# Kernel optimization log

Hardware: AMD Instinct MI355X
Metric: run time of the kernel (lower is better)

## Reference

```python
import jax, jax.numpy as jnp
import numpy as np
from jax import lax

N, C_IN, C_OUT = 1, 16, 32
D = W = H = 48
K = 9                      # num_points (snake kernel size)
CENTER = K // 2
EXTEND_SCOPE = 1.0
EPS = 1e-5
GN_GROUPS = C_OUT // 4
DN = ('NCDHW', 'OIDHW', 'NCDHW')


def conv3d(x, w, strides, padding):
    return lax.conv_general_dilated(x, w, strides, padding, dimension_numbers=DN)


def snake_cumsum(off):
    # off: [N, K, D, W, H]. Cumulative offsets outward from the center point,
    # center forced to 0 (matches the sequential loop in _coordinate_map_3D).
    lower = jnp.flip(jnp.cumsum(jnp.flip(off[:, :CENTER], 1), 1), 1)
    upper = jnp.cumsum(off[:, CENTER + 1:], 1)
    zero = jnp.zeros_like(off[:, :1])
    return jnp.concatenate([lower, zero, upper], axis=1)


def coordinate_map_morph0(off):
    # off: [N, 6K, D, W, H]; morph==0 uses z_offset1 (chans [0,K)) and y_offset1 ([K,2K)).
    cz = snake_cumsum(off[:, :K])
    cy = snake_cumsum(off[:, K:2 * K])
    dt = off.dtype
    zb = jnp.arange(D, dtype=dt)[None, None, :, None, None]
    yb = jnp.arange(W, dtype=dt)[None, None, None, :, None]
    xb = (jnp.arange(H, dtype=dt)[None, None, None, None, :]
          + (jnp.arange(K, dtype=dt) - CENTER)[None, :, None, None, None])
    z = zb + EXTEND_SCOPE * cz                      # [N,K,D,W,H]
    y = yb + EXTEND_SCOPE * cy
    x = jnp.broadcast_to(xb, z.shape)

    def rearr(c):  # [N,K,D,W,H] -> [N,D,W,H*K]  (h-major, k-minor, as in torch permute/reshape)
        return jnp.transpose(c, (0, 2, 3, 4, 1)).reshape(c.shape[0], D, W, H * K)

    return rearr(z), rearr(y), rearr(x)


def trilinear(feat, z, y, x):
    # feat [N,C,D,W,H]; z,y,x [N,D,W,H*K] float coords -> [N,C,D,W,H*K]
    z = jnp.clip(z, 0.0, D - 1.0)
    y = jnp.clip(y, 0.0, W - 1.0)
    x = jnp.clip(x, 0.0, H - 1.0)
    z0 = jnp.clip(jnp.floor(z).astype(jnp.int32), 0, D - 1); z1 = jnp.clip(z0 + 1, 0, D - 1)
    y0 = jnp.clip(jnp.floor(y).astype(jnp.int32), 0, W - 1); y1 = jnp.clip(y0 + 1, 0, W - 1)
    x0 = jnp.clip(jnp.floor(x).astype(jnp.int32), 0, H - 1); x1 = jnp.clip(x0 + 1, 0, H - 1)
    featl = jnp.transpose(feat, (0, 2, 3, 4, 1))  # [N,D,W,H,C]
    b = jnp.arange(feat.shape[0])[:, None, None, None]
    g = lambda zi, yi, xi: featl[b, zi, yi, xi]   # [N,D,W,H*K,C]
    f = feat.dtype
    wz0 = (z1.astype(f) - z)[..., None]; wz1 = (z - z0.astype(f))[..., None]
    wy0 = (y1.astype(f) - y)[..., None]; wy1 = (y - y0.astype(f))[..., None]
    wx0 = (x1.astype(f) - x)[..., None]; wx1 = (x - x0.astype(f))[..., None]
    out = (g(z0, y0, x0) * wz0 * wy0 * wx0 + g(z0, y0, x1) * wz0 * wy0 * wx1
         + g(z0, y1, x0) * wz0 * wy1 * wx0 + g(z0, y1, x1) * wz0 * wy1 * wx1
         + g(z1, y0, x0) * wz1 * wy0 * wx0 + g(z1, y0, x1) * wz1 * wy0 * wx1
         + g(z1, y1, x0) * wz1 * wy1 * wx0 + g(z1, y1, x1) * wz1 * wy1 * wx1)
    return jnp.transpose(out, (0, 4, 1, 2, 3))


def group_norm(x, gamma, beta):
    n = x.shape[0]
    xg = x.reshape(n, GN_GROUPS, -1)
    mu = xg.mean(-1, keepdims=True)
    var = xg.var(-1, keepdims=True)
    xg = (xg - mu) * lax.rsqrt(var + EPS)
    return xg.reshape(x.shape) * gamma[None, :, None, None, None] + beta[None, :, None, None, None]


def setup_inputs() -> dict:
    key = jax.random.key(0)
    ks = jax.random.split(key, 6)
    s = 0.05
    return {
        'x': jax.random.normal(ks[0], (N, C_IN, D, W, H), jnp.float32),
        'ow': jax.random.normal(ks[1], (6 * K, C_IN, 3, 3, 3), jnp.float32) * s,
        'ob': jax.random.normal(ks[2], (6 * K,), jnp.float32) * s,
        'bn_gamma': jnp.ones((6 * K,), jnp.float32),
        'bn_beta': jnp.zeros((6 * K,), jnp.float32),
        'bn_mean': jnp.zeros((6 * K,), jnp.float32),
        'bn_var': jnp.ones((6 * K,), jnp.float32),
        'dw': jax.random.normal(ks[3], (C_OUT, C_IN, 1, 1, K), jnp.float32) * s,
        'db': jax.random.normal(ks[4], (C_OUT,), jnp.float32) * s,
        'gn_gamma': jnp.ones((C_OUT,), jnp.float32),
        'gn_beta': jnp.zeros((C_OUT,), jnp.float32),
    }


def reference(x, ow, ob, bn_gamma, bn_beta, bn_mean, bn_var, dw, db, gn_gamma, gn_beta):
    # offset branch: conv3x3x3 -> BN (eval) -> tanh
    off = conv3d(x, ow, (1, 1, 1), 'SAME') + ob[None, :, None, None, None]
    c = lambda v: v[None, :, None, None, None]
    off = (off - c(bn_mean)) * lax.rsqrt(c(bn_var) + EPS) * c(bn_gamma) + c(bn_beta)
    off = jnp.tanh(off)
    # deformed sampling coordinates (morph 0: spread along x/height axis)
    zc, yc, xc = coordinate_map_morph0(off)
    deformed = trilinear(x, zc, yc, xc)           # [N,C,D,W,H*K]
    # snake conv: kernel (1,1,K) stride (1,1,K) -> [N,C_OUT,D,W,H]
    out = conv3d(deformed, dw, (1, 1, K), 'VALID') + db[None, :, None, None, None]
    out = group_norm(out, gn_gamma, gn_beta)
    return jax.nn.relu(out)
```

## Files before the change

### kernel.cpp

```cpp
#include <hip/hip_runtime.h>

#define DD    48
#define SP    (48*48*48)
#define CIN   16
#define KOFF  18
#define COUT  32
#define KK    9
#define NG    8
#define EPSV  1e-5f

__global__ __launch_bounds__(256) void k_zero(float* __restrict__ stats) {
    stats[threadIdx.x] = 0.0f;
}

__global__ __launch_bounds__(256) void k_xt(const float* __restrict__ x,
                                            float* __restrict__ xt) {
    int t = threadIdx.x;
    int vb = t >> 2, c = t & 3;
    int v = blockIdx.x * 64 + vb;
    float4 o;
    o.x = x[(4 * c + 0) * SP + v];
    o.y = x[(4 * c + 1) * SP + v];
    o.z = x[(4 * c + 2) * SP + v];
    o.w = x[(4 * c + 3) * SP + v];
    *reinterpret_cast<float4*>(xt + v * 16 + 4 * c) = o;
}

#define COH 9
__global__ __launch_bounds__(256) void k_offset(
    const float* __restrict__ xt, const float* __restrict__ ow,
    const float* __restrict__ ob, const float* __restrict__ bng,
    const float* __restrict__ bnb,const float* __restrict__ bnm,
    const float* __restrict__ bnv,float* __restrict__ off)
{
    const int cb = blockIdx.y * COH;
    __shared__ float wsm[27 * 4 * COH * 4];
    for (int i = threadIdx.x; i < 27 * CIN * COH; i += 256) {
        int co = i % COH; int r = i / COH; int ci = r % CIN; int tap = r / CIN;
        int c = ci >> 2, j = ci & 3;
        wsm[((tap * 4 + c) * COH + co) * 4 + j] = ow[((cb + co) * CIN + ci) * 27 + tap];
    }
    __syncthreads();

    const int t  = threadIdx.x;
    const int c  = t & 3;
    const int vb = t >> 2;
    const int v  = blockIdx.x * 64 + vb;
    const int h = v % DD, w = (v / DD) % DD, d = v / (DD * DD);

    float acc[COH];
#pragma unroll
    for (int co = 0; co < COH; ++co) acc[co] = 0.0f;

    const float* xc = xt + 4 * c;

#pragma unroll
    for (int kd = 0; kd < 3; ++kd) {
        int z = d + kd - 1; bool okz = (unsigned)z < (unsigned)DD;
#pragma unroll
        for (int kw = 0; kw < 3; ++kw) {
            int yy = w + kw - 1; bool oky = (unsigned)yy < (unsigned)DD;
#pragma unroll
            for (int kh = 0; kh < 3; ++kh) {
                int xx = h + kh - 1;
                if (okz && oky && (unsigned)xx < (unsigned)DD) {
                    int tap = (kd * 3 + kw) * 3 + kh;
                    float4 xv = *reinterpret_cast<const float4*>(
                        xc + ((z * DD + yy) * DD + xx) * 16);
                    const float4* wrow = reinterpret_cast<const float4*>(
                        &wsm[(tap * 4 + c) * COH * 4]);
#pragma unroll
                    for (int co = 0; co < COH; ++co) {
                        float4 w4 = wrow[co];
                        acc[co] += w4.x * xv.x + w4.y * xv.y
                                 + w4.z * xv.z + w4.w * xv.w;
                    }
                }
            }
        }
    }

#pragma unroll
    for (int co = 0; co < COH; ++co) {
        acc[co] += __shfl_xor(acc[co], 1);
        acc[co] += __shfl_xor(acc[co], 2);
    }

#pragma unroll
    for (int c0 = 0; c0 < 3; ++c0) {
        if (c == c0) {
#pragma unroll
            for (int j = 0; j < 3; ++j) {
                int co = c0 * 3 + j;
                int ch = cb + co;
                float scale = bng[ch] * rsqrtf(bnv[ch] + EPSV);
                float val   = (acc[co] + ob[ch] - bnm[ch]) * scale + bnb[ch];
                off[ch * SP + v] = tanhf(val);
            }
        }
    }
}

__global__ __launch_bounds__(256) void k_snake(
    const float* __restrict__ xt,  const float* __restrict__ off,
    const float* __restrict__ dw,  const float* __restrict__ db,
    float* __restrict__ pre,       float* __restrict__ stats)
{
    __shared__ float wl[KK * 4 * 132];
    __shared__ float lstat[16];
    for (int i = threadIdx.x; i < KK * CIN * COUT; i += 256) {
        int co = i % COUT; int r = i / COUT; int ci = r % CIN; int k = r / CIN;
        int c = ci >> 2, j = ci & 3;
        wl[(k * 4 + c) * 132 + co * 4 + j] = dw[(co * CIN + ci) * KK + k];
    }
    if (threadIdx.x < 16) lstat[threadIdx.x] = 0.0f;
    __syncthreads();

    const int nwg = SP / 64;
    int bid = (int)blockIdx.x;
    bid = (bid & 7) * (nwg >> 3) + (bid >> 3);

    const int t  = threadIdx.x;
    const int c  = t & 3;
    const int vb = t >> 2;
    const int v  = bid * 64 + vb;
    const int h = v % DD, w = (v / DD) % DD, d = v / (DD * DD);

    float acc[COUT];
#pragma unroll
    for (int co = 0; co < COUT; ++co) acc[co] = 0.0f;

    auto process = [&](int k, float czv, float cyv) {
        int xcol = h + k - 4;
        if (xcol >= DD - 1) return;
        if (xcol < 0) xcol = 0;

        float zf = fminf(fmaxf((float)d + czv, 0.0f), 47.0f);
        float yf = fminf(fmaxf((float)w + cyv, 0.0f), 47.0f);
        int z0 = (int)zf, y0 = (int)yf;
        int z1 = min(z0 + 1, 47), y1 = min(y0 + 1, 47);
        float wz1 = zf - (float)z0, wz0 = (float)z1 - zf;
        float wy1 = yf - (float)y0, wy0 = (float)y1 - yf;
        float w00 = wz0 * wy0, w01 = wz0 * wy1, w10 = wz1 * wy0, w11 = wz1 * wy1;

        const float* base = xt + 4 * c;
        float s0, s1, s2, s3;
        {
            const float4 A = *reinterpret_cast<const float4*>(base + ((z0 * DD + y0) * DD + xcol) * 16);
            const float4 B = *reinterpret_cast<const float4*>(base + ((z0 * DD + y1) * DD + xcol) * 16);
            s0 = w00 * A.x + w01 * B.x;
            s1 = w00 * A.y + w01 * B.y;
            s2 = w00 * A.z + w01 * B.z;
            s3 = w00 * A.w + w01 * B.w;
        }
        {
            const float4 C = *reinterpret_cast<const float4*>(base + ((z1 * DD + y0) * DD + xcol) * 16);
            const float4 E = *reinterpret_cast<const float4*>(base + ((z1 * DD + y1) * DD + xcol) * 16);
            s0 += w10 * C.x + w11 * E.x;
            s1 += w10 * C.y + w11 * E.y;
            s2 += w10 * C.z + w11 * E.z;
            s3 += w10 * C.w + w11 * E.w;
        }

        const float4* wrow = reinterpret_cast<const float4*>(&wl[(k * 4 + c) * 132]);
#pragma unroll
        for (int co = 0; co < COUT; ++co) {
            float4 w4 = wrow[co];
            acc[co] += w4.x * s0 + w4.y * s1 + w4.z * s2 + w4.w * s3;
        }
    };

    process(4, 0.0f, 0.0f);
    {
        float rz = 0.0f, ry = 0.0f;
#pragma unroll
        for (int k = 3; k >= 0; --k) {
            rz += off[k * SP + v];
            ry += off[(KK + k) * SP + v];
            process(k, rz, ry);
        }
    }
    {
        float rz = 0.0f, ry = 0.0f;
#pragma unroll
        for (int k = 5; k < KK; ++k) {
            rz += off[k * SP + v];
            ry += off[(KK + k) * SP + v];
            process(k, rz, ry);
        }
    }

#pragma unroll
    for (int co = 0; co < COUT; ++co) {
        acc[co] += __shfl_xor(acc[co], 1);
        acc[co] += __shfl_xor(acc[co], 2);
        acc[co] += db[co];
    }

#pragma unroll
    for (int cc = 0; cc < 4; ++cc) {
        if (c == cc) {
#pragma unroll
            for (int j = 0; j < 8; ++j)
                pre[(cc * 8 + j) * SP + v] = acc[cc * 8 + j];
        }
    }

#pragma unroll
    for (int g = 0; g < NG; ++g) {
        float a0 = acc[4*g], a1 = acc[4*g+1], a2 = acc[4*g+2], a3 = acc[4*g+3];
        float s  = a0 + a1 + a2 + a3;
        float ss = a0*a0 + a1*a1 + a2*a2 + a3*a3;
#pragma unroll
        for (int o = 4; o <= 32; o <<= 1) {
            s  += __shfl_xor(s,  o);
            ss += __shfl_xor(ss, o);
        }
        if ((t & 63) == 0) {
            atomicAdd(&lstat[g],      s);
            atomicAdd(&lstat[NG + g], ss);
        }
    }
    __syncthreads();
    if (t < 16) atomicAdd(&stats[t * 16], lstat[t]);
}

__global__ __launch_bounds__(256) void k_gn(
    float* __restrict__ buf, const float* __restrict__ stats,
    const float* __restrict__ gamma, const float* __restrict__ beta)
{
    int idx  = blockIdx.x * 256 + threadIdx.x;
    int base = idx * 4;
    int ch = base / SP, g = ch >> 2;

    const float inv_n = 1.0f / (4.0f * (float)SP);
    float mean = stats[g * 16] * inv_n;
    float var  = stats[(NG + g) * 16] * inv_n - mean * mean;
    float rs   = rsqrtf(var + EPSV);
    float ga   = gamma[ch] * rs;
    float be   = beta[ch] - mean * ga;

    float4 p = *reinterpret_cast<const float4*>(buf + base);
    float4 o;
    o.x = fmaxf(p.x * ga + be, 0.0f);
    o.y = fmaxf(p.y * ga + be, 0.0f);
    o.z = fmaxf(p.z * ga + be, 0.0f);
    o.w = fmaxf(p.w * ga + be, 0.0f);
    *reinterpret_cast<float4*>(buf + base) = o;
}

extern "C" void kernel_launch(void* const* d_in, const int* in_sizes, int n_in,
                              void* d_out, int out_size, void* d_ws, size_t ws_size,
                              hipStream_t stream)
{
    const float* x   = (const float*)d_in[0];
    const float* ow  = (const float*)d_in[1];
    const float* ob  = (const float*)d_in[2];
    const float* bng = (const float*)d_in[3];
    const float* bnb = (const float*)d_in[4];
    const float* bnm = (const float*)d_in[5];
    const float* bnv = (const float*)d_in[6];
    const float* dw  = (const float*)d_in[7];
    const float* db  = (const float*)d_in[8];
    const float* gng = (const float*)d_in[9];
    const float* gnb = (const float*)d_in[10];
    float* out = (float*)d_out;

    float* off   = (float*)d_ws;
    float* xt    = off + KOFF * SP;
    float* stats = xt + CIN * SP;

    k_zero  <<<1, 256, 0, stream>>>(stats);
    k_xt    <<<SP / 64, 256, 0, stream>>>(x, xt);
    k_offset<<<dim3(SP / 64, 2), 256, 0, stream>>>(xt, ow, ob, bng, bnb, bnm, bnv, off);
    k_snake <<<SP / 64, 256, 0, stream>>>(xt, off, dw, db, out, stats);
    k_gn    <<<(COUT * SP / 4) / 256, 256, 0, stream>>>(out, stats, gng, gnb);
}
```

Before: 224.7 us.

## Fuse offset conv with snake sampling to keep offsets in registers

Merges the offset convolution/BN/tanh kernel into the snake deformable-sampling kernel so the 18 offset channels stay in registers instead of going through a global workspace. Per-channel BN scale and shift are also precomputed once per block in shared memory. This removes the offset tensor's global write and read and one kernel launch. In exchange it raises register and LDS use per block, which may lower occupancy.

Result: slower. 283.0 us (+25.9%).

```diff
diff --git a/kernel.cpp b/kernel.cpp
--- a/kernel.cpp
+++ b/kernel.cpp
@@ -3,7 +3,6 @@
 #define DD    48
 #define SP    (48*48*48)
 #define CIN   16
-#define KOFF  18
 #define COUT  32
 #define KK    9
 #define NG    8
@@ -26,33 +25,53 @@
     *reinterpret_cast<float4*>(xt + v * 16 + 4 * c) = o;
 }
 
-#define COH 9
-__global__ __launch_bounds__(256) void k_offset(
-    const float* __restrict__ xt, const float* __restrict__ ow,
-    const float* __restrict__ ob, const float* __restrict__ bng,
-    const float* __restrict__ bnb,const float* __restrict__ bnm,
-    const float* __restrict__ bnv,float* __restrict__ off)
+__global__ __launch_bounds__(256) void k_fused(
+    const float* __restrict__ xt,  const float* __restrict__ ow,
+    const float* __restrict__ ob,  const float* __restrict__ bng,
+    const float* __restrict__ bnb, const float* __restrict__ bnm,
+    const float* __restrict__ bnv, const float* __restrict__ dw,
+    const float* __restrict__ db,  float* __restrict__ pre,
+    float* __restrict__ stats)
 {
-    const int cb = blockIdx.y * COH;
-    __shared__ float wsm[27 * 4 * COH * 4];
-    for (int i = threadIdx.x; i < 27 * CIN * COH; i += 256) {
-        int co = i % COH; int r = i / COH; int ci = r % CIN; int tap = r / CIN;
+    __shared__ float cw[27 * 4 * 72];
+    __shared__ float wl[KK * 4 * 132];
+    __shared__ float bnsc[18], bnsh[18];
+    __shared__ float lstat[16];
+
+    for (int i = threadIdx.x; i < 27 * CIN * 18; i += 256) {
+        int ch = i % 18; int r = i / 18; int ci = r % CIN; int tap = r / CIN;
         int c = ci >> 2, j = ci & 3;
-        wsm[((tap * 4 + c) * COH + co) * 4 + j] = ow[((cb + co) * CIN + ci) * 27 + tap];
-    }
+        cw[(tap * 4 + c) * 72 + ch * 4 + j] = ow[(ch * CIN + ci) * 27 + tap];
+    }
+    for (int i = threadIdx.x; i < KK * CIN * COUT; i += 256) {
+        int co = i % COUT; int r = i / COUT; int ci = r % CIN; int k = r / CIN;
+        int c = ci >> 2, j = ci & 3;
+        wl[(k * 4 + c) * 132 + co * 4 + j] = dw[(co * CIN + ci) * KK + k];
+    }
+    if (threadIdx.x < 18) {
+        int ch = threadIdx.x;
+        float sc = bng[ch] * rsqrtf(bnv[ch] + EPSV);
+        bnsc[ch] = sc;
+        bnsh[ch] = (ob[ch] - bnm[ch]) * sc + bnb[ch];
+    }
+    if (threadIdx.x < 16) lstat[threadIdx.x] = 0.0f;
     __syncthreads();
+
+    const int nwg = SP / 64;
+    int bid = (int)blockIdx.x;
+    bid = (bid & 7) * (nwg >> 3) + (bid >> 3);
 
     const int t  = threadIdx.x;
     const int c  = t & 3;
     const int vb = t >> 2;
-    const int v  = blockIdx.x * 64 + vb;
+    const int v  = bid * 64 + vb;
     const int h = v % DD, w = (v / DD) % DD, d = v / (DD * DD);
 
-    float acc[COH];
-#pragma unroll
-    for (int co = 0; co < COH; ++co) acc[co] = 0.0f;
-
     const float* xc = xt + 4 * c;
+
+    float a18[18];
+#pragma unroll
+    for (int co = 0; co < 18; ++co) a18[co] = 0.0f;
 
 #pragma unroll
     for (int kd = 0; kd < 3; ++kd) {
@@ -68,11 +87,11 @@
                     float4 xv = *reinterpret_cast<const float4*>(
                         xc + ((z * DD + yy) * DD + xx) * 16);
                     const float4* wrow = reinterpret_cast<const float4*>(
-                        &wsm[(tap * 4 + c) * COH * 4]);
-#pragma unroll
-                    for (int co = 0; co < COH; ++co) {
+                        &cw[(tap * 4 + c) * 72]);
+#pragma unroll
+                    for (int co = 0; co < 18; ++co) {
                         float4 w4 = wrow[co];
-                        acc[co] += w4.x * xv.x + w4.y * xv.y
+                        a18[co] += w4.x * xv.x + w4.y * xv.y
                                  + w4.z * xv.z + w4.w * xv.w;
                     }
                 }
@@ -81,50 +100,11 @@
     }
 
 #pragma unroll
-    for (int co = 0; co < COH; ++co) {
-        acc[co] += __shfl_xor(acc[co], 1);
-        acc[co] += __shfl_xor(acc[co], 2);
-    }
-
-#pragma unroll
-    for (int c0 = 0; c0 < 3; ++c0) {
-        if (c == c0) {
-#pragma unroll
-            for (int j = 0; j < 3; ++j) {
-                int co = c0 * 3 + j;
-                int ch = cb + co;
-                float scale = bng[ch] * rsqrtf(bnv[ch] + EPSV);
-                float val   = (acc[co] + ob[ch] - bnm[ch]) * scale + bnb[ch];
-                off[ch * SP + v] = tanhf(val);
-            }
-        }
-    }
-}
-
-__global__ __launch_bounds__(256) void k_snake(
-    const float* __restrict__ xt,  const float* __restrict__ off,
-    const float* __restrict__ dw,  const float* __restrict__ db,
-    float* __restrict__ pre,       float* __restrict__ stats)
-{
-    __shared__ float wl[KK * 4 * 132];
-    __shared__ float lstat[16];
-    for (int i = threadIdx.x; i < KK * CIN * COUT; i += 256) {
-        int co = i % COUT; int r = i / COUT; int ci = r % CIN; int k = r / CIN;
-        int c = ci >> 2, j = ci & 3;
-        wl[(k * 4 + c) * 132 + co * 4 + j] = dw[(co * CIN + ci) * KK + k];
-    }
-    if (threadIdx.x < 16) lstat[threadIdx.x] = 0.0f;
-    __syncthreads();
-
-    const int nwg = SP / 64;
-    int bid = (int)blockIdx.x;
-    bid = (bid & 7) * (nwg >> 3) + (bid >> 3);
-
-    const int t  = threadIdx.x;
-    const int c  = t & 3;
-    const int vb = t >> 2;
-    const int v  = bid * 64 + vb;
-    const int h = v % DD, w = (v / DD) % DD, d = v / (DD * DD);
+    for (int co = 0; co < 18; ++co) {
+        a18[co] += __shfl_xor(a18[co], 1);
+        a18[co] += __shfl_xor(a18[co], 2);
+        a18[co] = tanhf(a18[co] * bnsc[co] + bnsh[co]);
+    }
 
     float acc[COUT];
 #pragma unroll
@@ -175,8 +155,8 @@
         float rz = 0.0f, ry = 0.0f;
 #pragma unroll
         for (int k = 3; k >= 0; --k) {
-            rz += off[k * SP + v];
-            ry += off[(KK + k) * SP + v];
+            rz += a18[k];
+            ry += a18[KK + k];
             process(k, rz, ry);
         }
     }
@@ -184,8 +164,8 @@
         float rz = 0.0f, ry = 0.0f;
 #pragma unroll
         for (int k = 5; k < KK; ++k) {
-            rz += off[k * SP + v];
-            ry += off[(KK + k) * SP + v];
+            rz += a18[k];
+            ry += a18[KK + k];
             process(k, rz, ry);
         }
     }
@@ -266,13 +246,12 @@
     const float* gnb = (const float*)d_in[10];
     float* out = (float*)d_out;
 
-    float* off   = (float*)d_ws;
-    float* xt    = off + KOFF * SP;
+    float* xt    = (float*)d_ws;
     float* stats = xt + CIN * SP;
 
-    k_zero  <<<1, 256, 0, stream>>>(stats);
-    k_xt    <<<SP / 64, 256, 0, stream>>>(x, xt);
-    k_offset<<<dim3(SP / 64, 2), 256, 0, stream>>>(xt, ow, ob, bng, bnb, bnm, bnv, off);
-    k_snake <<<SP / 64, 256, 0, stream>>>(xt, off, dw, db, out, stats);
-    k_gn    <<<(COUT * SP / 4) / 256, 256, 0, stream>>>(out, stats, gng, gnb);
-}
+    k_zero <<<1, 256, 0, stream>>>(stats);
+    k_xt   <<<SP / 64, 256, 0, stream>>>(x, xt);
+    k_fused<<<SP / 64, 256, 0, stream>>>(xt, ow, ob, bng, bnb, bnm, bnv,
+                                         dw, db, out, stats);
+    k_gn   <<<(COUT * SP / 4) / 256, 256, 0, stream>>>(out, stats, gng, gnb);
+}
```
